# Kernel tuning notes

Measured on AMD Instinct MI355X. Metric: run time of the kernel, lower is better.

The kernel has to match this reference:

```python
import jax, jax.numpy as jnp
import numpy as np

STRIDE = 1
PADDING = 3
DILATION = 1


def setup_inputs() -> dict:
    key = jax.random.key(0)
    k1, k2 = jax.random.split(key)
    B, C, H, W = 8, 512, 64, 64
    G, K = 8, 7
    Ho, Wo = H // STRIDE, W // STRIDE
    x = jax.random.normal(k1, (B, C, H, W), dtype=jnp.float32)
    weight = jax.random.normal(k2, (B, G, K, K, Ho, Wo), dtype=jnp.float32)
    return {"x": x, "weight": weight}


def reference(x, weight):
    # x: [B, C, H, W]; weight: [B, G, K, K, Ho, Wo]
    B, C, H, W = x.shape
    _, G, K, _, Ho, Wo = weight.shape
    cpg = C // G  # channels per group
    # zero-pad spatial dims (matches CUDA boundary check)
    xp = jnp.pad(x, ((0, 0), (0, 0), (PADDING, PADDING), (PADDING, PADDING)))
    out = jnp.zeros((B, G, cpg, Ho, Wo), dtype=x.dtype)
    for kh in range(K):
        for kw in range(K):
            h0 = kh * DILATION
            w0 = kw * DILATION
            # strided window: input pixel h*stride - pad + kh*dil for each output h
            patch = xp[:, :,
                       h0:h0 + (Ho - 1) * STRIDE + 1:STRIDE,
                       w0:w0 + (Wo - 1) * STRIDE + 1:STRIDE]  # [B, C, Ho, Wo]
            wk = weight[:, :, kh, kw]  # [B, G, Ho, Wo]
            out = out + patch.reshape(B, G, cpg, Ho, Wo) * wk[:, :, None]
    return out.reshape(B, C, Ho, Wo)
```

## Files before the change

kernel.cpp:

```cpp
#include <hip/hip_runtime.h>


#define BB 8
#define CC 512
#define GG 8
#define CPG 64
#define HH 64
#define WW 64
#define HW (HH * WW)
#define KK 7
#define PAD 3

#define TILE_ROWS 8
#define CSPLIT 16
#define CHPC 4
#define LDS_ROWS (TILE_ROWS + KK - 1)
#define LDS_PITCH 72
#define CH_STRIDE (LDS_ROWS * LDS_PITCH)
#define NQUADS (LDS_ROWS * (LDS_PITCH / 4))

__global__ __launch_bounds__(256, 8)
void involution_kernel(const float* __restrict__ x,
                       const float* __restrict__ weight,
                       float* __restrict__ out) {
    const int tid = threadIdx.x;
    const int tx = tid & 31;
    const int ty = tid >> 5;

    const int f = blockIdx.x;
    const int xcd = f & 7;
    const int k = f >> 3;
    const int bg = ((k >> 7) << 3) + xcd;
    const int sub = k & 127;
    const int b = bg >> 3;
    const int g = bg & 7;
    const int tile = sub >> 4;
    const int cs = sub & 15;

    const int wo0 = tx << 1;
    const int hbase = tile * TILE_ROWS;
    const int ho = hbase + ty;

    __shared__ float xs[CHPC * CH_STRIDE];

    const float* wq = weight + ((size_t)(b * GG + g) * (KK * KK)) * HW
                    + ho * WW + wo0;

    const int sr = tid / 18;
    const int sq = tid - sr * 18;
    const int xrow = hbase + sr - PAD;
    const int xcol = sq * 4 - 4;
    const bool sval = (tid < NQUADS)
                   && ((unsigned)xrow < HH) && ((unsigned)xcol < WW);
    const int soff = xrow * WW + xcol;
    const int ldsoff = sr * LDS_PITCH + sq * 4;

    const size_t cbase = (size_t)(b * CC + g * CPG + cs * CHPC) * HW;
    const float* xg = x + cbase;
    float* og = out + cbase + ho * WW + wo0;

    float4 q[CHPC];
#pragma unroll
    for (int ch = 0; ch < CHPC; ++ch) {
        float4 v = make_float4(0.f, 0.f, 0.f, 0.f);
        if (sval)
            v = *(const float4*)(xg + (size_t)ch * HW + soff);
        q[ch] = v;
    }
    if (tid < NQUADS) {
#pragma unroll
        for (int ch = 0; ch < CHPC; ++ch)
            *(float4*)(&xs[ch * CH_STRIDE + ldsoff]) = q[ch];
    }
    __syncthreads();

    float acc0[CHPC], acc1[CHPC];
#pragma unroll
    for (int ch = 0; ch < CHPC; ++ch) { acc0[ch] = 0.f; acc1[ch] = 0.f; }

#pragma unroll
    for (int kh = 0; kh < KK; ++kh) {
        __builtin_amdgcn_sched_barrier(0);
        float2 wk[KK];
#pragma unroll
        for (int j = 0; j < KK; ++j)
            wk[j] = *(const float2*)(wq + (size_t)(kh * KK + j) * HW);

#pragma unroll
        for (int ch = 0; ch < CHPC; ++ch) {
            const float* row = &xs[ch * CH_STRIDE + (ty + kh) * LDS_PITCH + wo0];
            const float2 p0 = *(const float2*)(row + 0);
            const float2 p1 = *(const float2*)(row + 2);
            const float2 p2 = *(const float2*)(row + 4);
            const float2 p3 = *(const float2*)(row + 6);
            const float2 p4 = *(const float2*)(row + 8);
            const float f1 = p0.y, f2 = p1.x, f3 = p1.y, f4 = p2.x;
            const float f5 = p2.y, f6 = p3.x, f7 = p3.y, f8 = p4.x;
            float a0 = acc0[ch], a1 = acc1[ch];
            a0 = fmaf(f1, wk[0].x, a0);  a1 = fmaf(f2, wk[0].y, a1);
            a0 = fmaf(f2, wk[1].x, a0);  a1 = fmaf(f3, wk[1].y, a1);
            a0 = fmaf(f3, wk[2].x, a0);  a1 = fmaf(f4, wk[2].y, a1);
            a0 = fmaf(f4, wk[3].x, a0);  a1 = fmaf(f5, wk[3].y, a1);
            a0 = fmaf(f5, wk[4].x, a0);  a1 = fmaf(f6, wk[4].y, a1);
            a0 = fmaf(f6, wk[5].x, a0);  a1 = fmaf(f7, wk[5].y, a1);
            a0 = fmaf(f7, wk[6].x, a0);  a1 = fmaf(f8, wk[6].y, a1);
            acc0[ch] = a0; acc1[ch] = a1;
        }
    }

#pragma unroll
    for (int ch = 0; ch < CHPC; ++ch) {
        *(float2*)(og + (size_t)ch * HW)
            = make_float2(acc0[ch], acc1[ch]);
    }
}

extern "C" void kernel_launch(void* const* d_in, const int* in_sizes, int n_in,
                              void* d_out, int out_size, void* d_ws, size_t ws_size,
                              hipStream_t stream) {
    const float* x = (const float*)d_in[0];
    const float* w = (const float*)d_in[1];
    float* out = (float*)d_out;

    dim3 grid((HH / TILE_ROWS) * CSPLIT * GG * BB);
    dim3 block(256);
    involution_kernel<<<grid, block, 0, stream>>>(x, w, out);
}
```

Measured before the change: 208.2 us.

## Compute four output columns per thread over 16-row tiles

Each thread now produces four adjacent output columns instead of two, and each block covers 16 output rows instead of 8. The input halo staging loop is generalised to spread all channel planes across threads in several passes. This amortises LDS reads and weight loads over more outputs and cuts the halo overhead per tile. In exchange it uses more registers per thread, lowers the occupancy hint to 4, and halves the grid size.

Result: faster. 195.3 us (-6.2%).

```diff
diff --git a/kernel.cpp b/kernel.cpp
--- a/kernel.cpp
+++ b/kernel.cpp
@@ -11,33 +11,35 @@
 #define KK 7
 #define PAD 3
 
-#define TILE_ROWS 8
+#define TILE_ROWS 16
 #define CSPLIT 16
 #define CHPC 4
 #define LDS_ROWS (TILE_ROWS + KK - 1)
 #define LDS_PITCH 72
 #define CH_STRIDE (LDS_ROWS * LDS_PITCH)
-#define NQUADS (LDS_ROWS * (LDS_PITCH / 4))
+#define PLANE_QUADS (LDS_ROWS * (LDS_PITCH / 4))
+#define TOT_QUADS (CHPC * PLANE_QUADS)
+#define NPASS ((TOT_QUADS + 255) / 256)
 
-__global__ __launch_bounds__(256, 8)
+__global__ __launch_bounds__(256, 4)
 void involution_kernel(const float* __restrict__ x,
                        const float* __restrict__ weight,
                        float* __restrict__ out) {
     const int tid = threadIdx.x;
-    const int tx = tid & 31;
-    const int ty = tid >> 5;
+    const int tx = tid & 15;
+    const int ty = tid >> 4;
 
     const int f = blockIdx.x;
     const int xcd = f & 7;
     const int k = f >> 3;
-    const int bg = ((k >> 7) << 3) + xcd;
-    const int sub = k & 127;
+    const int bg = ((k >> 6) << 3) + xcd;
+    const int sub = k & 63;
     const int b = bg >> 3;
     const int g = bg & 7;
     const int tile = sub >> 4;
     const int cs = sub & 15;
 
-    const int wo0 = tx << 1;
+    const int wo0 = tx << 2;
     const int hbase = tile * TILE_ROWS;
     const int ho = hbase + ty;
 
@@ -46,73 +48,82 @@
     const float* wq = weight + ((size_t)(b * GG + g) * (KK * KK)) * HW
                     + ho * WW + wo0;
 
-    const int sr = tid / 18;
-    const int sq = tid - sr * 18;
-    const int xrow = hbase + sr - PAD;
-    const int xcol = sq * 4 - 4;
-    const bool sval = (tid < NQUADS)
-                   && ((unsigned)xrow < HH) && ((unsigned)xcol < WW);
-    const int soff = xrow * WW + xcol;
-    const int ldsoff = sr * LDS_PITCH + sq * 4;
-
     const size_t cbase = (size_t)(b * CC + g * CPG + cs * CHPC) * HW;
     const float* xg = x + cbase;
     float* og = out + cbase + ho * WW + wo0;
 
-    float4 q[CHPC];
+    {
+        float4 sv[NPASS];
+        int lofs[NPASS];
+        bool act[NPASS];
 #pragma unroll
-    for (int ch = 0; ch < CHPC; ++ch) {
-        float4 v = make_float4(0.f, 0.f, 0.f, 0.f);
-        if (sval)
-            v = *(const float4*)(xg + (size_t)ch * HW + soff);
-        q[ch] = v;
-    }
-    if (tid < NQUADS) {
+        for (int i = 0; i < NPASS; ++i) {
+            const int q = tid + i * 256;
+            act[i] = (q < TOT_QUADS);
+            const int p = q / PLANE_QUADS;
+            const int r = q - p * PLANE_QUADS;
+            const int sr = r / 18;
+            const int sq = r - sr * 18;
+            const int xrow = hbase + sr - PAD;
+            const int xcol = (sq << 2) - 4;
+            const bool ld = act[i]
+                         && ((unsigned)xrow < HH) && ((unsigned)xcol < WW);
+            float4 v = make_float4(0.f, 0.f, 0.f, 0.f);
+            if (ld)
+                v = *(const float4*)(xg + (size_t)p * HW + xrow * WW + xcol);
+            sv[i] = v;
+            lofs[i] = p * CH_STRIDE + sr * LDS_PITCH + (sq << 2);
+        }
 #pragma unroll
-        for (int ch = 0; ch < CHPC; ++ch)
-            *(float4*)(&xs[ch * CH_STRIDE + ldsoff]) = q[ch];
+        for (int i = 0; i < NPASS; ++i)
+            if (act[i]) *(float4*)(&xs[lofs[i]]) = sv[i];
     }
     __syncthreads();
 
-    float acc0[CHPC], acc1[CHPC];
+    float4 acc[CHPC];
 #pragma unroll
-    for (int ch = 0; ch < CHPC; ++ch) { acc0[ch] = 0.f; acc1[ch] = 0.f; }
+    for (int ch = 0; ch < CHPC; ++ch)
+        acc[ch] = make_float4(0.f, 0.f, 0.f, 0.f);
 
 #pragma unroll
     for (int kh = 0; kh < KK; ++kh) {
         __builtin_amdgcn_sched_barrier(0);
-        float2 wk[KK];
+        float4 wk[KK];
 #pragma unroll
         for (int j = 0; j < KK; ++j)
-            wk[j] = *(const float2*)(wq + (size_t)(kh * KK + j) * HW);
+            wk[j] = *(const float4*)(wq + (size_t)(kh * KK + j) * HW);
 
 #pragma unroll
         for (int ch = 0; ch < CHPC; ++ch) {
-            const float* row = &xs[ch * CH_STRIDE + (ty + kh) * LDS_PITCH + wo0];
-            const float2 p0 = *(const float2*)(row + 0);
-            const float2 p1 = *(const float2*)(row + 2);
-            const float2 p2 = *(const float2*)(row + 4);
-            const float2 p3 = *(const float2*)(row + 6);
-            const float2 p4 = *(const float2*)(row + 8);
-            const float f1 = p0.y, f2 = p1.x, f3 = p1.y, f4 = p2.x;
-            const float f5 = p2.y, f6 = p3.x, f7 = p3.y, f8 = p4.x;
-            float a0 = acc0[ch], a1 = acc1[ch];
-            a0 = fmaf(f1, wk[0].x, a0);  a1 = fmaf(f2, wk[0].y, a1);
-            a0 = fmaf(f2, wk[1].x, a0);  a1 = fmaf(f3, wk[1].y, a1);
-            a0 = fmaf(f3, wk[2].x, a0);  a1 = fmaf(f4, wk[2].y, a1);
-            a0 = fmaf(f4, wk[3].x, a0);  a1 = fmaf(f5, wk[3].y, a1);
-            a0 = fmaf(f5, wk[4].x, a0);  a1 = fmaf(f6, wk[4].y, a1);
-            a0 = fmaf(f6, wk[5].x, a0);  a1 = fmaf(f7, wk[5].y, a1);
-            a0 = fmaf(f7, wk[6].x, a0);  a1 = fmaf(f8, wk[6].y, a1);
-            acc0[ch] = a0; acc1[ch] = a1;
+            const float* rowp = &xs[ch * CH_STRIDE + (ty + kh) * LDS_PITCH + wo0];
+            const float4 x0 = *(const float4*)(rowp);
+            const float4 x1 = *(const float4*)(rowp + 4);
+            const float4 x2 = *(const float4*)(rowp + 8);
+            const float w1 = x0.y, w2 = x0.z, w3 = x0.w;
+            const float w4 = x1.x, w5 = x1.y, w6 = x1.z, w7 = x1.w;
+            const float w8 = x2.x, w9 = x2.y, w10 = x2.z;
+            float4 a = acc[ch];
+            a.x = fmaf(w1, wk[0].x, a.x);  a.y = fmaf(w2, wk[0].y, a.y);
+            a.z = fmaf(w3, wk[0].z, a.z);  a.w = fmaf(w4, wk[0].w, a.w);
+            a.x = fmaf(w2, wk[1].x, a.x);  a.y = fmaf(w3, wk[1].y, a.y);
+            a.z = fmaf(w4, wk[1].z, a.z);  a.w = fmaf(w5, wk[1].w, a.w);
+            a.x = fmaf(w3, wk[2].x, a.x);  a.y = fmaf(w4, wk[2].y, a.y);
+            a.z = fmaf(w5, wk[2].z, a.z);  a.w = fmaf(w6, wk[2].w, a.w);
+            a.x = fmaf(w4, wk[3].x, a.x);  a.y = fmaf(w5, wk[3].y, a.y);
+            a.z = fmaf(w6, wk[3].z, a.z);  a.w = fmaf(w7, wk[3].w, a.w);
+            a.x = fmaf(w5, wk[4].x, a.x);  a.y = fmaf(w6, wk[4].y, a.y);
+            a.z = fmaf(w7, wk[4].z, a.z);  a.w = fmaf(w8, wk[4].w, a.w);
+            a.x = fmaf(w6, wk[5].x, a.x);  a.y = fmaf(w7, wk[5].y, a.y);
+            a.z = fmaf(w8, wk[5].z, a.z);  a.w = fmaf(w9, wk[5].w, a.w);
+            a.x = fmaf(w7, wk[6].x, a.x);  a.y = fmaf(w8, wk[6].y, a.y);
+            a.z = fmaf(w9, wk[6].z, a.z);  a.w = fmaf(w10, wk[6].w, a.w);
+            acc[ch] = a;
         }
     }
 
 #pragma unroll
-    for (int ch = 0; ch < CHPC; ++ch) {
-        *(float2*)(og + (size_t)ch * HW)
-            = make_float2(acc0[ch], acc1[ch]);
-    }
+    for (int ch = 0; ch < CHPC; ++ch)
+        *(float4*)(og + (size_t)ch * HW) = acc[ch];
 }
 
 extern "C" void kernel_launch(void* const* d_in, const int* in_sizes, int n_in,
```
